# Optimization experiments

Measured on AMD Instinct MI355X. Metric: run time of the kernel, lower is better.

## Reference

```python
import jax, jax.numpy as jnp
import numpy as np

N = 50000      # nodes
E = 800000     # edges per edge type
T = 2          # edge types
IN = 128       # in_feats
H = 4          # num_heads
DH = 32        # out_feats // num_heads
OUT = H * DH   # out_feats
EPS = 1e-12
NEG_SLOPE = 0.2


def setup_inputs() -> dict:
    key = jax.random.key(0)
    ks = jax.random.split(key, 10)
    feature = jax.random.normal(ks[0], (N, IN), dtype=jnp.float32)
    src = jax.random.randint(ks[1], (T, E), 0, N, dtype=jnp.int32)
    dst = jax.random.randint(ks[2], (T, E), 0, N, dtype=jnp.int32)
    # GATConv parameters per edge type (xavier-ish init scale)
    W = jax.random.normal(ks[3], (T, IN, OUT), dtype=jnp.float32) * (1.0 / np.sqrt(IN))
    attn_l = jax.random.normal(ks[4], (T, H, DH), dtype=jnp.float32) * 0.1
    attn_r = jax.random.normal(ks[5], (T, H, DH), dtype=jnp.float32) * 0.1
    bias = jnp.zeros((T, OUT), dtype=jnp.float32)
    ln_w = jnp.ones((T, OUT), dtype=jnp.float32)
    ln_b = jnp.zeros((T, OUT), dtype=jnp.float32)
    return {"feature": feature, "src": src, "dst": dst, "W": W,
            "attn_l": attn_l, "attn_r": attn_r, "bias": bias,
            "ln_w": ln_w, "ln_b": ln_b}


def _gat_edge_type(feature, W_t, al_t, ar_t, b_t, lw_t, lb_t, src_t, dst_t):
    # fc projection: [N, H, DH]
    fh = (feature @ W_t).reshape(N, H, DH)
    el = jnp.sum(fh * al_t, axis=-1)            # [N, H]
    er = jnp.sum(fh * ar_t, axis=-1)            # [N, H]
    e = jax.nn.leaky_relu(el[src_t] + er[dst_t], NEG_SLOPE)  # [E, H]
    # segment softmax over destination nodes (stable)
    m = jax.ops.segment_max(e, dst_t, num_segments=N)        # [N, H]
    a = jnp.exp(e - jax.lax.stop_gradient(m)[dst_t])         # [E, H]
    den = jax.ops.segment_sum(a, dst_t, num_segments=N)      # [N, H]
    alpha = a / den[dst_t]                                   # [E, H]
    msg = fh[src_t] * alpha[:, :, None]                      # [E, H, DH]
    agg = jax.ops.segment_sum(msg, dst_t, num_segments=N)    # [N, H, DH]
    h = agg.reshape(N, OUT) + b_t                            # flatten + bias
    # LayerNorm (biased variance, eps inside sqrt) as in source
    u = jnp.mean(h, axis=-1, keepdims=True)
    s = jnp.mean((h - u) ** 2, axis=-1, keepdims=True)
    h = lw_t * ((h - u) / jnp.sqrt(s + EPS)) + lb_t
    return jax.nn.elu(h)                                     # activation (dropout p=0)


def reference(feature, src, dst, W, attn_l, attn_r, bias, ln_w, ln_b):
    hidden = [
        _gat_edge_type(feature, W[t], attn_l[t], attn_r[t], bias[t],
                       ln_w[t], ln_b[t], src[t], dst[t])
        for t in range(T)
    ]
    return jnp.stack(hidden, axis=1)  # [N, T, OUT]
```

## Files before the change

### kernel.cpp

```cpp
#include <hip/hip_runtime.h>
#include <math.h>

#define NN 50000
#define EE 800000
#define TT 2
#define HH 4
#define OUTF 128

constexpr float NEG_SLOPE = 0.2f;
constexpr float LN_EPS = 1e-12f;

#define GM 64
#define KB 32
#define APAD 36
#define WPAD 132

__global__ __launch_bounds__(256) void gemm_fh_elr(const float* __restrict__ A,
                                                   const float* __restrict__ W,
                                                   const float* __restrict__ al,
                                                   const float* __restrict__ ar,
                                                   float* __restrict__ fh,
                                                   float* __restrict__ el,
                                                   float* __restrict__ er) {
  __shared__ float As[GM][APAD];
  __shared__ float Ws[KB][WPAD];
  const int t = blockIdx.y;
  const int row0 = blockIdx.x * GM;
  const int tid = threadIdx.x;
  const int tcol = tid & 15;
  const int trow = tid >> 4;
  const float* Wt = W + (size_t)t * 128 * 128;

  float acc[4][8];
#pragma unroll
  for (int i = 0; i < 4; ++i)
#pragma unroll
    for (int j = 0; j < 8; ++j) acc[i][j] = 0.f;

  for (int kk = 0; kk < 128; kk += KB) {
#pragma unroll
    for (int j = 0; j < 2; ++j) {
      int f = tid + 256 * j;
      int r = f >> 3, kq = f & 7;
      int grow = row0 + r;
      float4 v = make_float4(0.f, 0.f, 0.f, 0.f);
      if (grow < NN) v = *(const float4*)(A + (size_t)grow * 128 + kk + kq * 4);
      *(float4*)&As[r][kq * 4] = v;
    }
#pragma unroll
    for (int j = 0; j < 4; ++j) {
      int f = tid + 256 * j;
      int kq = f >> 5, c4 = f & 31;
      float4 v = *(const float4*)(Wt + (size_t)(kk + kq) * 128 + c4 * 4);
      *(float4*)&Ws[kq][c4 * 4] = v;
    }
    __syncthreads();
#pragma unroll
    for (int k = 0; k < KB; ++k) {
      float a0 = As[4 * trow + 0][k];
      float a1 = As[4 * trow + 1][k];
      float a2 = As[4 * trow + 2][k];
      float a3 = As[4 * trow + 3][k];
      float4 b0 = *(const float4*)&Ws[k][4 * tcol];
      float4 b1 = *(const float4*)&Ws[k][64 + 4 * tcol];
      acc[0][0] += a0 * b0.x; acc[0][1] += a0 * b0.y; acc[0][2] += a0 * b0.z; acc[0][3] += a0 * b0.w;
      acc[0][4] += a0 * b1.x; acc[0][5] += a0 * b1.y; acc[0][6] += a0 * b1.z; acc[0][7] += a0 * b1.w;
      acc[1][0] += a1 * b0.x; acc[1][1] += a1 * b0.y; acc[1][2] += a1 * b0.z; acc[1][3] += a1 * b0.w;
      acc[1][4] += a1 * b1.x; acc[1][5] += a1 * b1.y; acc[1][6] += a1 * b1.z; acc[1][7] += a1 * b1.w;
      acc[2][0] += a2 * b0.x; acc[2][1] += a2 * b0.y; acc[2][2] += a2 * b0.z; acc[2][3] += a2 * b0.w;
      acc[2][4] += a2 * b1.x; acc[2][5] += a2 * b1.y; acc[2][6] += a2 * b1.z; acc[2][7] += a2 * b1.w;
      acc[3][0] += a3 * b0.x; acc[3][1] += a3 * b0.y; acc[3][2] += a3 * b0.z; acc[3][3] += a3 * b0.w;
      acc[3][4] += a3 * b1.x; acc[3][5] += a3 * b1.y; acc[3][6] += a3 * b1.z; acc[3][7] += a3 * b1.w;
    }
    __syncthreads();
  }
#pragma unroll
  for (int i = 0; i < 4; ++i) {
    int grow = row0 + 4 * trow + i;
    if (grow < NN) {
      float* o = fh + ((size_t)t * NN + grow) * 128;
      *(float4*)(o + 4 * tcol) = make_float4(acc[i][0], acc[i][1], acc[i][2], acc[i][3]);
      *(float4*)(o + 64 + 4 * tcol) = make_float4(acc[i][4], acc[i][5], acc[i][6], acc[i][7]);
    }
  }
  const int ha = tcol >> 3;
  const int ci = (4 * tcol) & 31;
  float4 alA = *(const float4*)(al + (size_t)(t * HH + ha) * 32 + ci);
  float4 arA = *(const float4*)(ar + (size_t)(t * HH + ha) * 32 + ci);
  float4 alB = *(const float4*)(al + (size_t)(t * HH + 2 + ha) * 32 + ci);
  float4 arB = *(const float4*)(ar + (size_t)(t * HH + 2 + ha) * 32 + ci);
#pragma unroll
  for (int i = 0; i < 4; ++i) {
    float pla = acc[i][0] * alA.x + acc[i][1] * alA.y + acc[i][2] * alA.z + acc[i][3] * alA.w;
    float pra = acc[i][0] * arA.x + acc[i][1] * arA.y + acc[i][2] * arA.z + acc[i][3] * arA.w;
    float plb = acc[i][4] * alB.x + acc[i][5] * alB.y + acc[i][6] * alB.z + acc[i][7] * alB.w;
    float prb = acc[i][4] * arB.x + acc[i][5] * arB.y + acc[i][6] * arB.z + acc[i][7] * arB.w;
#pragma unroll
    for (int off = 1; off <= 4; off <<= 1) {
      pla += __shfl_xor(pla, off, 64);
      pra += __shfl_xor(pra, off, 64);
      plb += __shfl_xor(plb, off, 64);
      prb += __shfl_xor(prb, off, 64);
    }
    if ((tcol & 7) == 0) {
      int row = row0 + 4 * trow + i;
      if (row < NN) {
        size_t base = ((size_t)t * NN + row) * HH;
        el[base + ha] = pla;
        er[base + ha] = pra;
        el[base + 2 + ha] = plb;
        er[base + 2 + ha] = prb;
      }
    }
  }
}

__global__ __launch_bounds__(256) void build_list(const int* __restrict__ src,
                                                  const int* __restrict__ dst,
                                                  int* __restrict__ head,
                                                  int2* __restrict__ rec) {
  const int t = blockIdx.y;
  int i4 = (blockIdx.x * 256 + threadIdx.x) * 4;
  if (i4 >= EE) return;
  int2* recT = rec + (size_t)t * EE;
  int* headT = head + t * NN;
  if (i4 + 3 < EE) {
    int4 d = *(const int4*)(dst + (size_t)t * EE + i4);
    int4 s = *(const int4*)(src + (size_t)t * EE + i4);
    int o0 = atomicExch(&headT[d.x], i4 + 0);
    int o1 = atomicExch(&headT[d.y], i4 + 1);
    int o2 = atomicExch(&headT[d.z], i4 + 2);
    int o3 = atomicExch(&headT[d.w], i4 + 3);
    *(int4*)&recT[i4] = make_int4(o0, s.x, o1, s.y);
    *(int4*)&recT[i4 + 2] = make_int4(o2, s.z, o3, s.w);
  } else {
    for (int j = 0; j < 4 && i4 + j < EE; ++j) {
      int d = dst[(size_t)t * EE + i4 + j];
      int s = src[(size_t)t * EE + i4 + j];
      int o = atomicExch(&headT[d], i4 + j);
      recT[i4 + j] = make_int2(o, s);
    }
  }
}

__global__ __launch_bounds__(256) void gat_node(const float* __restrict__ fh,
                                                const float* __restrict__ el,
                                                const float* __restrict__ er,
                                                const int* __restrict__ head,
                                                const int2* __restrict__ rec,
                                                const float* __restrict__ bias,
                                                const float* __restrict__ lnw,
                                                const float* __restrict__ lnb,
                                                float* __restrict__ out) {
  const int item = blockIdx.x * 8 + (threadIdx.x >> 5);
  const int t = item / NN;
  const int n = item % NN;
  const int l = threadIdx.x & 31;
  const int c0 = 4 * l;
  const int h = l >> 3;

  const int2* recT = rec + (size_t)t * EE;
  const float* elp = el + (size_t)t * NN * HH;
  const float* fhp = fh + (size_t)t * NN * 128;
  const float erh = er[((size_t)t * NN + n) * HH + h];

  float den = 0.f;
  float ax = 0.f, ay = 0.f, az = 0.f, aw = 0.f;
  int e = head[t * NN + n];
  while (e >= 0) {
    int2 r = recT[e];
    int s = r.y;
    float x = elp[(size_t)s * HH + h] + erh;
    x = (x > 0.f) ? x : NEG_SLOPE * x;
    float a = __expf(x);
    den += a;
    float4 f = *(const float4*)(fhp + (size_t)s * 128 + c0);
    ax += a * f.x; ay += a * f.y; az += a * f.z; aw += a * f.w;
    e = r.x;
  }
  float inv = (den > 0.f) ? 1.f / den : 0.f;
  float hx = ax * inv + bias[t * OUTF + c0 + 0];
  float hy = ay * inv + bias[t * OUTF + c0 + 1];
  float hz = az * inv + bias[t * OUTF + c0 + 2];
  float hw = aw * inv + bias[t * OUTF + c0 + 3];

  float s1 = hx + hy + hz + hw;
#pragma unroll
  for (int off = 16; off >= 1; off >>= 1) s1 += __shfl_xor(s1, off, 32);
  float u = s1 * (1.f / OUTF);
  float dx = hx - u, dy = hy - u, dz = hz - u, dw = hw - u;
  float s2 = dx * dx + dy * dy + dz * dz + dw * dw;
#pragma unroll
  for (int off = 16; off >= 1; off >>= 1) s2 += __shfl_xor(s2, off, 32);
  float rstd = rsqrtf(s2 * (1.f / OUTF) + LN_EPS);

  float4 wv = *(const float4*)(lnw + t * OUTF + c0);
  float4 bv = *(const float4*)(lnb + t * OUTF + c0);
  float y0 = wv.x * (dx * rstd) + bv.x;
  float y1 = wv.y * (dy * rstd) + bv.y;
  float y2 = wv.z * (dz * rstd) + bv.z;
  float y3 = wv.w * (dw * rstd) + bv.w;
  y0 = (y0 > 0.f) ? y0 : expm1f(y0);
  y1 = (y1 > 0.f) ? y1 : expm1f(y1);
  y2 = (y2 > 0.f) ? y2 : expm1f(y2);
  y3 = (y3 > 0.f) ? y3 : expm1f(y3);

  *(float4*)(out + ((size_t)n * TT + t) * OUTF + c0) = make_float4(y0, y1, y2, y3);
}

extern "C" void kernel_launch(void* const* d_in, const int* in_sizes, int n_in,
                              void* d_out, int out_size, void* d_ws, size_t ws_size,
                              hipStream_t stream) {
  const float* feature = (const float*)d_in[0];
  const int* src = (const int*)d_in[1];
  const int* dst = (const int*)d_in[2];
  const float* W = (const float*)d_in[3];
  const float* al = (const float*)d_in[4];
  const float* ar = (const float*)d_in[5];
  const float* bias = (const float*)d_in[6];
  const float* lnw = (const float*)d_in[7];
  const float* lnb = (const float*)d_in[8];
  float* out = (float*)d_out;

  char* ws = (char*)d_ws;
  size_t off = 0;
  auto carve = [&](size_t bytes) -> void* {
    void* p = ws + off;
    off += (bytes + 511) & ~(size_t)511;
    return p;
  };
  float* fh = (float*)carve((size_t)TT * NN * 128 * 4);
  float* el = (float*)carve((size_t)TT * NN * HH * 4);
  float* er = (float*)carve((size_t)TT * NN * HH * 4);
  int* head = (int*)carve((size_t)TT * NN * 4);
  int2* rec = (int2*)carve((size_t)TT * EE * 8);

  hipMemsetAsync(head, 0xFF, (size_t)TT * NN * 4, stream);

  gemm_fh_elr<<<dim3((NN + GM - 1) / GM, TT), 256, 0, stream>>>(feature, W, al, ar, fh, el, er);
  build_list<<<dim3((EE / 4 + 255) / 256, TT), 256, 0, stream>>>(src, dst, head, rec);
  gat_node<<<(TT * NN) / 8, 256, 0, stream>>>(fh, el, er, head, rec,
                                              bias, lnw, lnb, out);
}
```

Before: 364.4 us.

## Split edge lists into two chains and embed el values in edge records

Each destination now gets two linked lists, chosen by edge index parity, so the node kernel can walk two chains at once and overlap their dependent loads. Edge records grow to 32 bytes and carry the source's four el values, which removes one dependent gather per edge in the node kernel. The cost is larger record writes and an el gather inside build_list. That kernel now has to run after the GEMM, and the record array doubles the memory traffic.

After: 358.8 us. No clear change (-1.5%).

```diff
diff --git a/kernel.cpp b/kernel.cpp
--- a/kernel.cpp
+++ b/kernel.cpp
@@ -117,37 +117,34 @@
 
 __global__ __launch_bounds__(256) void build_list(const int* __restrict__ src,
                                                   const int* __restrict__ dst,
+                                                  const float* __restrict__ el,
                                                   int* __restrict__ head,
-                                                  int2* __restrict__ rec) {
+                                                  float* __restrict__ rec) {
   const int t = blockIdx.y;
   int i4 = (blockIdx.x * 256 + threadIdx.x) * 4;
   if (i4 >= EE) return;
-  int2* recT = rec + (size_t)t * EE;
-  int* headT = head + t * NN;
-  if (i4 + 3 < EE) {
-    int4 d = *(const int4*)(dst + (size_t)t * EE + i4);
-    int4 s = *(const int4*)(src + (size_t)t * EE + i4);
-    int o0 = atomicExch(&headT[d.x], i4 + 0);
-    int o1 = atomicExch(&headT[d.y], i4 + 1);
-    int o2 = atomicExch(&headT[d.z], i4 + 2);
-    int o3 = atomicExch(&headT[d.w], i4 + 3);
-    *(int4*)&recT[i4] = make_int4(o0, s.x, o1, s.y);
-    *(int4*)&recT[i4 + 2] = make_int4(o2, s.z, o3, s.w);
-  } else {
-    for (int j = 0; j < 4 && i4 + j < EE; ++j) {
-      int d = dst[(size_t)t * EE + i4 + j];
-      int s = src[(size_t)t * EE + i4 + j];
-      int o = atomicExch(&headT[d], i4 + j);
-      recT[i4 + j] = make_int2(o, s);
-    }
+  float* recT = rec + (size_t)t * EE * 8;
+  int* headT = head + (size_t)t * NN * 2;
+  const float* elT = el + (size_t)t * NN * HH;
+#pragma unroll
+  for (int j = 0; j < 4; ++j) {
+    int i = i4 + j;
+    if (i >= EE) break;
+    int d = dst[(size_t)t * EE + i];
+    int s = src[(size_t)t * EE + i];
+    float4 ev = *(const float4*)(elT + (size_t)s * HH);
+    int o = atomicExch(&headT[d * 2 + (i & 1)], i);
+    float* r = recT + (size_t)i * 8;
+    int4 w0 = make_int4(o, s, __float_as_int(ev.x), __float_as_int(ev.y));
+    *(int4*)r = w0;
+    *(float2*)(r + 4) = make_float2(ev.z, ev.w);
   }
 }
 
 __global__ __launch_bounds__(256) void gat_node(const float* __restrict__ fh,
-                                                const float* __restrict__ el,
                                                 const float* __restrict__ er,
                                                 const int* __restrict__ head,
-                                                const int2* __restrict__ rec,
+                                                const float* __restrict__ rec,
                                                 const float* __restrict__ bias,
                                                 const float* __restrict__ lnw,
                                                 const float* __restrict__ lnb,
@@ -159,25 +156,53 @@
   const int c0 = 4 * l;
   const int h = l >> 3;
 
-  const int2* recT = rec + (size_t)t * EE;
-  const float* elp = el + (size_t)t * NN * HH;
+  const float* recT = rec + (size_t)t * EE * 8;
   const float* fhp = fh + (size_t)t * NN * 128;
   const float erh = er[((size_t)t * NN + n) * HH + h];
 
+  int2 hh = *(const int2*)(head + ((size_t)t * NN + n) * 2);
+  int e0 = hh.x, e1 = hh.y;
+
   float den = 0.f;
   float ax = 0.f, ay = 0.f, az = 0.f, aw = 0.f;
-  int e = head[t * NN + n];
+
+  while (e0 >= 0 && e1 >= 0) {
+    const float* p0 = recT + (size_t)e0 * 8;
+    const float* p1 = recT + (size_t)e1 * 8;
+    int2 ns0 = *(const int2*)p0;
+    int2 ns1 = *(const int2*)p1;
+    float el0 = p0[2 + h];
+    float el1 = p1[2 + h];
+    float4 f0 = *(const float4*)(fhp + (size_t)ns0.y * 128 + c0);
+    float4 f1 = *(const float4*)(fhp + (size_t)ns1.y * 128 + c0);
+    float x0 = el0 + erh;
+    float x1 = el1 + erh;
+    x0 = (x0 > 0.f) ? x0 : NEG_SLOPE * x0;
+    x1 = (x1 > 0.f) ? x1 : NEG_SLOPE * x1;
+    float a0 = __expf(x0);
+    float a1 = __expf(x1);
+    den += a0 + a1;
+    ax += a0 * f0.x + a1 * f1.x;
+    ay += a0 * f0.y + a1 * f1.y;
+    az += a0 * f0.z + a1 * f1.z;
+    aw += a0 * f0.w + a1 * f1.w;
+    e0 = ns0.x;
+    e1 = ns1.x;
+  }
+  int e = (e0 >= 0) ? e0 : e1;
   while (e >= 0) {
-    int2 r = recT[e];
-    int s = r.y;
-    float x = elp[(size_t)s * HH + h] + erh;
+    const float* pe = recT + (size_t)e * 8;
+    int2 ns = *(const int2*)pe;
+    float elh = pe[2 + h];
+    float4 f = *(const float4*)(fhp + (size_t)ns.y * 128 + c0);
+    float x = elh + erh;
     x = (x > 0.f) ? x : NEG_SLOPE * x;
     float a = __expf(x);
     den += a;
-    float4 f = *(const float4*)(fhp + (size_t)s * 128 + c0);
     ax += a * f.x; ay += a * f.y; az += a * f.z; aw += a * f.w;
-    e = r.x;
-  }
+    e = ns.x;
+  }
+
   float inv = (den > 0.f) ? 1.f / den : 0.f;
   float hx = ax * inv + bias[t * OUTF + c0 + 0];
   float hy = ay * inv + bias[t * OUTF + c0 + 1];
@@ -232,13 +257,13 @@
   float* fh = (float*)carve((size_t)TT * NN * 128 * 4);
   float* el = (float*)carve((size_t)TT * NN * HH * 4);
   float* er = (float*)carve((size_t)TT * NN * HH * 4);
-  int* head = (int*)carve((size_t)TT * NN * 4);
-  int2* rec = (int2*)carve((size_t)TT * EE * 8);
-
-  hipMemsetAsync(head, 0xFF, (size_t)TT * NN * 4, stream);
+  int* head = (int*)carve((size_t)TT * NN * 2 * 4);
+  float* rec = (float*)carve((size_t)TT * EE * 32);
+
+  hipMemsetAsync(head, 0xFF, (size_t)TT * NN * 2 * 4, stream);
 
   gemm_fh_elr<<<dim3((NN + GM - 1) / GM, TT), 256, 0, stream>>>(feature, W, al, ar, fh, el, er);
-  build_list<<<dim3((EE / 4 + 255) / 256, TT), 256, 0, stream>>>(src, dst, head, rec);
-  gat_node<<<(TT * NN) / 8, 256, 0, stream>>>(fh, el, er, head, rec,
+  build_list<<<dim3((EE / 4 + 255) / 256, TT), 256, 0, stream>>>(src, dst, el, head, rec);
+  gat_node<<<(TT * NN) / 8, 256, 0, stream>>>(fh, er, head, rec,
                                               bias, lnw, lnb, out);
 }
```
